# Kernel optimization log

Measured on AMD Instinct MI355X. Metric: run time of the kernel, lower is better.

## Reference

```python
import jax, jax.numpy as jnp
import numpy as np

B, T, N, F, H, E = 8, 16, 10000, 64, 64, 1000000
M = B * N  # flattened node count per timestep
NUM_CLASSES = 3


def setup_inputs() -> dict:
    key = jax.random.key(0)
    ks = jax.random.split(key, 10)
    s = 1.0 / np.sqrt(H)
    return {
        "graph_seq": jax.random.normal(ks[0], (B, T, N, F), dtype=jnp.float32),
        "edge_index_seq": jax.random.randint(ks[1], (T, 2, E), 0, M, dtype=jnp.int32),
        "W_gcn": jax.random.normal(ks[2], (F, H), dtype=jnp.float32) / np.sqrt(F),
        "b_gcn": jnp.zeros((H,), dtype=jnp.float32),
        "W_ih": jax.random.uniform(ks[3], (4 * H, H), jnp.float32, -s, s),
        "W_hh": jax.random.uniform(ks[4], (4 * H, H), jnp.float32, -s, s),
        "b_ih": jax.random.uniform(ks[5], (4 * H,), jnp.float32, -s, s),
        "b_hh": jax.random.uniform(ks[6], (4 * H,), jnp.float32, -s, s),
        "W_fc": jax.random.uniform(ks[7], (NUM_CLASSES, H), jnp.float32, -s, s),
        "b_fc": jax.random.uniform(ks[8], (NUM_CLASSES,), jnp.float32, -s, s),
    }


def _forward(graph_seq, edge_index_seq, W_gcn, b_gcn, W_ih, W_hh, b_ih, b_hh, W_fc, b_fc):
    # GCNConv: x' = D^{-1/2}(A+I)D^{-1/2} (x W) + b, applied on flattened (B*N) nodes per timestep.
    xw = jnp.einsum('btnf,fh->btnh', graph_seq, W_gcn)        # [B,T,N,H]
    xw_t = xw.transpose(1, 0, 2, 3).reshape(T, M, H)          # [T, B*N, H], node index = b*N + n

    def gcn_step(_, inp):
        x, ei = inp                                           # x: [M,H], ei: [2,E]
        src, dst = ei[0], ei[1]
        deg = jax.ops.segment_sum(jnp.ones((E,), x.dtype), dst, num_segments=M) + 1.0  # +1 self loop
        dinv = jax.lax.rsqrt(deg)
        coef = dinv[src] * dinv[dst]                          # [E]
        agg = jax.ops.segment_sum(x[src] * coef[:, None], dst, num_segments=M)
        out = agg + x * (dinv * dinv)[:, None] + b_gcn        # self-loop term + bias
        pooled = out.reshape(B, N, H).mean(axis=1)            # mean over nodes -> [B,H]
        return None, pooled

    _, pooled_seq = jax.lax.scan(gcn_step, None, (xw_t, edge_index_seq))  # [T,B,H]

    def lstm_step(carry, x_t):
        h, c = carry
        z = x_t @ W_ih.T + h @ W_hh.T + b_ih + b_hh           # [B,4H], gate order i,f,g,o
        i, f, g, o = jnp.split(z, 4, axis=-1)
        c = jax.nn.sigmoid(f) * c + jax.nn.sigmoid(i) * jnp.tanh(g)
        h = jax.nn.sigmoid(o) * jnp.tanh(c)
        return (h, c), None

    h0 = jnp.zeros((B, H), dtype=graph_seq.dtype)
    (h_last, _), _ = jax.lax.scan(lstm_step, (h0, h0), pooled_seq)
    return h_last @ W_fc.T + b_fc                             # [B,3]


def reference(graph_seq, edge_index_seq, W_gcn, b_gcn, W_ih, W_hh, b_ih, b_hh, W_fc, b_fc):
    return _forward(graph_seq, edge_index_seq, W_gcn, b_gcn, W_ih, W_hh, b_ih, b_hh, W_fc, b_fc)
```

## Files before the change

kernel.cpp:

```cpp
#include <hip/hip_runtime.h>
#include <hip/hip_bf16.h>

#define BB 8
#define TT 16
#define NNODE 10000
#define FF 64
#define HH 64
#define EE 1000000
#define MM 80000
#define NCLS 3

#define NCHUNK 32
#define NPC 2500
#define CAPB 36032
#define NSEG_H 16
#define HW 20000
#define NSEG_B 32
#define EPW 7816
#define WCAP 144
#define FLUSH_THR 96
#define GPAD 16

__global__ __launch_bounds__(256) void k_hist(const int* __restrict__ ei,
                                              unsigned int* __restrict__ part, int t0) {
    __shared__ unsigned int h[HW];
    int seg = blockIdx.x, tloc = blockIdx.y, tg = t0 + tloc;
    for (int i = threadIdx.x; i < HW; i += 256) h[i] = 0u;
    __syncthreads();
    const uint4* dstp = (const uint4*)(ei + (size_t)tg * 2 * EE + EE
                                       + (size_t)seg * (EE / NSEG_H));
    for (int i = threadIdx.x; i < (EE / NSEG_H) / 4; i += 256) {
        uint4 d4 = dstp[i];
        atomicAdd(&h[d4.x >> 2], 1u << ((d4.x & 3u) * 8u));
        atomicAdd(&h[d4.y >> 2], 1u << ((d4.y & 3u) * 8u));
        atomicAdd(&h[d4.z >> 2], 1u << ((d4.z & 3u) * 8u));
        atomicAdd(&h[d4.w >> 2], 1u << ((d4.w & 3u) * 8u));
    }
    __syncthreads();
    unsigned int* outp = part + ((size_t)tloc * NSEG_H + seg) * HW;
    for (int i = threadIdx.x; i < HW; i += 256) outp[i] = h[i];
}

__global__ __launch_bounds__(256) void k_mdeg(const unsigned int* __restrict__ part,
                                              float* __restrict__ dinv) {
    int w = blockIdx.x * 256 + threadIdx.x;
    int tloc = blockIdx.y;
    if (w >= HW) return;
    const unsigned int* p = part + (size_t)tloc * NSEG_H * HW;
    unsigned int s = 0;
#pragma unroll
    for (int k = 0; k < NSEG_H; k++) s += p[(size_t)k * HW + w];
    float4 r;
    r.x = rsqrtf((float)(s & 255u) + 1.0f);
    r.y = rsqrtf((float)((s >> 8) & 255u) + 1.0f);
    r.z = rsqrtf((float)((s >> 16) & 255u) + 1.0f);
    r.w = rsqrtf((float)((s >> 24) & 255u) + 1.0f);
    *(float4*)(dinv + (size_t)tloc * MM + (size_t)w * 4) = r;
}

__global__ __launch_bounds__(256) void k_part(const int* __restrict__ ei,
                                              unsigned int* __restrict__ buck,
                                              unsigned int* __restrict__ gcur, int t0) {
    __shared__ unsigned int stg[4][NCHUNK][WCAP];
    __shared__ unsigned int cur[4][NCHUNK];
    int wave = threadIdx.x >> 6, lane = threadIdx.x & 63;
    int tloc = blockIdx.y, tg = t0 + tloc;
    if (lane < NCHUNK) cur[wave][lane] = 0u;

    int wseg = blockIdx.x * 4 + wave;
    int e0 = wseg * EPW;
    int e1 = e0 + EPW; if (e1 > EE) e1 = EE;
    const uint4* src4 = (const uint4*)(ei + (size_t)tg * 2 * EE);
    const uint4* dst4 = (const uint4*)(ei + (size_t)tg * 2 * EE + EE);
    unsigned int* gc = gcur + (size_t)tloc * NCHUNK * GPAD;
    unsigned int* bk = buck + (size_t)tloc * NCHUNK * CAPB;

    int i40 = e0 >> 2, i41 = e1 >> 2;
    int nIter = (i41 - i40 + 63) >> 6;
    for (int k = 0; k < nIter; k++) {
        int i4 = i40 + k * 64 + lane;
        if (i4 < i41) {
            uint4 s4 = src4[i4];
            uint4 d4 = dst4[i4];
            unsigned int ss[4] = {s4.x, s4.y, s4.z, s4.w};
            unsigned int dd[4] = {d4.x, d4.y, d4.z, d4.w};
#pragma unroll
            for (int j = 0; j < 4; j++) {
                unsigned int ck = (unsigned int)(((unsigned long long)ss[j] * 1717987ull) >> 32);
                unsigned int so = ss[j] - ck * NPC;
                unsigned int p = atomicAdd(&cur[wave][ck], 1u);
                if (p < WCAP) stg[wave][ck][p] = (so << 17) | dd[j];
            }
        }
        unsigned int cnt = (lane < NCHUNK) ? cur[wave][lane] : 0u;
        unsigned long long mask = __ballot(cnt >= FLUSH_THR);
        while (mask) {
            int ck = __ffsll((unsigned long long)mask) - 1;
            mask &= mask - 1;
            unsigned int n = cur[wave][ck];
            if (n > WCAP) n = WCAP;
            unsigned int gp = 0;
            if (lane == 0) gp = atomicAdd(&gc[ck * GPAD], n);
            gp = (unsigned int)__shfl((int)gp, 0);
            if (gp + n <= CAPB) {
                for (unsigned int j = lane; j < n; j += 64)
                    bk[(size_t)ck * CAPB + gp + j] = stg[wave][ck][j];
            }
            if (lane == 0) cur[wave][ck] = 0u;
        }
    }
    for (int ck = 0; ck < NCHUNK; ck++) {
        unsigned int n = cur[wave][ck];
        if (n > WCAP) n = WCAP;
        if (n > 0u) {
            unsigned int gp = 0;
            if (lane == 0) gp = atomicAdd(&gc[ck * GPAD], n);
            gp = (unsigned int)__shfl((int)gp, 0);
            if (gp + n <= CAPB) {
                for (unsigned int j = lane; j < n; j += 64)
                    bk[(size_t)ck * CAPB + gp + j] = stg[wave][ck][j];
            }
        }
    }
}

__global__ __launch_bounds__(512) void k_scat(const float* __restrict__ g,
                                              const float* __restrict__ dinv,
                                              const unsigned int* __restrict__ buck,
                                              const unsigned int* __restrict__ gcur,
                                              float* __restrict__ yp, int t0) {
    __shared__ float a[NPC * BB];
    int c = blockIdx.x, tloc = blockIdx.y, tg = t0 + tloc;
    for (int i = threadIdx.x; i < NPC * BB; i += 512) a[i] = 0.0f;
    __syncthreads();

    const float* dv = dinv + (size_t)tloc * MM;
    unsigned int n = gcur[((size_t)tloc * NCHUNK + c) * GPAD];
    if (n > CAPB) n = CAPB;
    const unsigned int* bk = buck + ((size_t)tloc * NCHUNK + c) * CAPB;

    unsigned int n4 = n >> 2;
    for (unsigned int i = threadIdx.x; i < n4; i += 512) {
        uint4 r = ((const uint4*)bk)[i];
        unsigned int rec[4] = {r.x, r.y, r.z, r.w};
#pragma unroll
        for (int k = 0; k < 4; k++) {
            unsigned int d = rec[k] & 0x1FFFFu;
            unsigned int so = rec[k] >> 17;
            unsigned int b = (unsigned int)(((unsigned long long)d * 429497ull) >> 32);
            atomicAdd(&a[so * BB + b], dv[d]);
        }
    }
    {
        unsigned int i = (n4 << 2) + threadIdx.x;
        if (i < n) {
            unsigned int rec = bk[i];
            unsigned int d = rec & 0x1FFFFu;
            unsigned int so = rec >> 17;
            unsigned int b = (unsigned int)(((unsigned long long)d * 429497ull) >> 32);
            atomicAdd(&a[so * BB + b], dv[d]);
        }
    }
    __syncthreads();

    int lane = threadIdx.x & 63;
    int wave = threadIdx.x >> 6;
    int sub = lane >> 4;
    int f0 = (lane & 15) << 2;
    int b_c = c >> 2;
    const size_t base_g = ((size_t)(b_c * TT + tg) * NNODE + (size_t)(c & 3) * NPC) * FF;
    const float* dvc = dv + (size_t)c * NPC;

    float acc[BB][4];
#pragma unroll
    for (int b = 0; b < BB; b++)
#pragma unroll
        for (int q = 0; q < 4; q++) acc[b][q] = 0.0f;

    const int NG = NPC / 4;
    for (int gi = wave; gi < NG; gi += 16) {
        int j0 = gi * 4 + sub;
        int gi1 = gi + 8;
        int j1 = gi1 * 4 + sub;
        bool has1 = (gi1 < NG);
        const float4 g40 = *(const float4*)(g + base_g + (size_t)j0 * FF + f0);
        float4 g41 = has1 ? *(const float4*)(g + base_g + (size_t)j1 * FF + f0)
                          : make_float4(0.f, 0.f, 0.f, 0.f);
        {
            float dvj = dvc[j0];
            const float4 a0 = *(const float4*)(&a[j0 * BB]);
            const float4 a1 = *(const float4*)(&a[j0 * BB + 4]);
            float av[BB] = {a0.x, a0.y, a0.z, a0.w, a1.x, a1.y, a1.z, a1.w};
#pragma unroll
            for (int b = 0; b < BB; b++) {
                float wv = dvj * (av[b] + (b == b_c ? dvj : 0.0f));
                acc[b][0] = fmaf(g40.x, wv, acc[b][0]);
                acc[b][1] = fmaf(g40.y, wv, acc[b][1]);
                acc[b][2] = fmaf(g40.z, wv, acc[b][2]);
                acc[b][3] = fmaf(g40.w, wv, acc[b][3]);
            }
        }
        if (has1) {
            float dvj = dvc[j1];
            const float4 a0 = *(const float4*)(&a[j1 * BB]);
            const float4 a1 = *(const float4*)(&a[j1 * BB + 4]);
            float av[BB] = {a0.x, a0.y, a0.z, a0.w, a1.x, a1.y, a1.z, a1.w};
#pragma unroll
            for (int b = 0; b < BB; b++) {
                float wv = dvj * (av[b] + (b == b_c ? dvj : 0.0f));
                acc[b][0] = fmaf(g41.x, wv, acc[b][0]);
                acc[b][1] = fmaf(g41.y, wv, acc[b][1]);
                acc[b][2] = fmaf(g41.z, wv, acc[b][2]);
                acc[b][3] = fmaf(g41.w, wv, acc[b][3]);
            }
        }
    }

    __syncthreads();
#pragma unroll
    for (int b = 0; b < BB; b++)
#pragma unroll
        for (int q = 0; q < 4; q++) {
            float v = acc[b][q];
            v += __shfl_xor(v, 16);
            v += __shfl_xor(v, 32);
            acc[b][q] = v;
        }
    if (sub == 0) {
#pragma unroll
        for (int b = 0; b < BB; b++)
#pragma unroll
            for (int q = 0; q < 4; q++)
                a[wave * (BB * FF) + b * FF + f0 + q] = acc[b][q];
    }
    __syncthreads();
    for (int idx = threadIdx.x; idx < BB * FF; idx += 512) {
        float s = 0.0f;
#pragma unroll
        for (int w = 0; w < 8; w++) s += a[w * (BB * FF) + idx];
        yp[((size_t)tg * NCHUNK + c) * (BB * FF) + idx] = s;
    }
}

__global__ __launch_bounds__(256) void k_lstm(const float* __restrict__ yp,
                                              const float* __restrict__ Wg,
                                              const float* __restrict__ bg,
                                              const float* __restrict__ Wih,
                                              const float* __restrict__ Whh,
                                              const float* __restrict__ bih,
                                              const float* __restrict__ bhh,
                                              const float* __restrict__ Wfc,
                                              const float* __restrict__ bfc,
                                              float* __restrict__ out) {
    int b = blockIdx.x;
    int r = threadIdx.x;

    __shared__ float ys[TT][FF];
    __shared__ float xs[TT][HH];
    __shared__ float hs[HH], cs[HH], zs[4 * HH];

    for (int idx = r; idx < TT * FF; idx += 256) {
        int t = idx >> 6, f = idx & 63;
        const float* p = yp + ((size_t)t * NCHUNK * BB + b) * FF + f;
        float s = 0.0f;
#pragma unroll
        for (int c = 0; c < NCHUNK; c++) s += p[(size_t)c * BB * FF];
        ys[t][f] = s;
    }
    __syncthreads();

    for (int idx = r; idx < TT * HH; idx += 256) {
        int t = idx >> 6, h = idx & 63;
        float s = 0.0f;
#pragma unroll
        for (int f = 0; f < FF; f++) s = fmaf(ys[t][f], Wg[f * HH + h], s);
        xs[t][h] = s * (1.0f / NNODE) + bg[h];
    }

    float wih[HH], whh[HH];
#pragma unroll
    for (int k = 0; k < HH; k++) {
        wih[k] = Wih[r * HH + k];
        whh[k] = Whh[r * HH + k];
    }
    float bias = bih[r] + bhh[r];

    if (r < HH) { hs[r] = 0.0f; cs[r] = 0.0f; }
    __syncthreads();

    for (int t = 0; t < TT; t++) {
        float acc = bias;
#pragma unroll
        for (int k = 0; k < HH; k++)
            acc = fmaf(wih[k], xs[t][k], fmaf(whh[k], hs[k], acc));
        zs[r] = acc;
        __syncthreads();
        if (r < HH) {
            float iv = zs[r], fv = zs[HH + r], gv = zs[2 * HH + r], ov = zs[3 * HH + r];
            float si = 1.0f / (1.0f + expf(-iv));
            float sf = 1.0f / (1.0f + expf(-fv));
            float so = 1.0f / (1.0f + expf(-ov));
            float cc = sf * cs[r] + si * tanhf(gv);
            cs[r] = cc;
            hs[r] = so * tanhf(cc);
        }
        __syncthreads();
    }

    if (r < NCLS) {
        float s = bfc[r];
#pragma unroll
        for (int k = 0; k < HH; k++) s = fmaf(hs[k], Wfc[r * HH + k], s);
        out[b * NCLS + r] = s;
    }
}

extern "C" void kernel_launch(void* const* d_in, const int* in_sizes, int n_in,
                              void* d_out, int out_size, void* d_ws, size_t ws_size,
                              hipStream_t stream) {
    const float* g   = (const float*)d_in[0];
    const int*   ei  = (const int*)d_in[1];
    const float* Wg  = (const float*)d_in[2];
    const float* bg  = (const float*)d_in[3];
    const float* Wih = (const float*)d_in[4];
    const float* Whh = (const float*)d_in[5];
    const float* bih = (const float*)d_in[6];
    const float* bhh = (const float*)d_in[7];
    const float* Wfc = (const float*)d_in[8];
    const float* bfc = (const float*)d_in[9];
    float* out = (float*)d_out;

    char* ws = (char*)d_ws;
    float* yp = (float*)ws;
    const size_t ypBytes = (size_t)TT * NCHUNK * BB * FF * sizeof(float);

    const size_t sz_dinv = (size_t)MM * 4;
    const size_t sz_part = (size_t)NSEG_H * HW * 4;
    const size_t sz_buck = (size_t)NCHUNK * CAPB * 4;
    const size_t sz_gcur = (size_t)NCHUNK * GPAD * 4;
    const size_t per_t = sz_dinv + sz_part + sz_buck + sz_gcur;

    size_t avail = (ws_size > ypBytes) ? ws_size - ypBytes : 0;
    int Tg = (int)(avail / per_t);
    if (Tg > TT) Tg = TT;
    if (Tg < 1) Tg = 1;

    float* dinv        = (float*)(ws + ypBytes);
    unsigned int* part = (unsigned int*)(ws + ypBytes + (size_t)Tg * sz_dinv);
    unsigned int* buck = (unsigned int*)(ws + ypBytes + (size_t)Tg * (sz_dinv + sz_part));
    unsigned int* gcur = (unsigned int*)(ws + ypBytes + (size_t)Tg * (sz_dinv + sz_part + sz_buck));

    for (int t0 = 0; t0 < TT; t0 += Tg) {
        int tc = (TT - t0 < Tg) ? (TT - t0) : Tg;
        hipMemsetAsync(gcur, 0, (size_t)tc * NCHUNK * GPAD * 4, stream);

        dim3 gh(NSEG_H, tc);
        k_hist<<<gh, 256, 0, stream>>>(ei, part, t0);

        dim3 gm((HW + 255) / 256, tc);
        k_mdeg<<<gm, 256, 0, stream>>>(part, dinv);

        dim3 gp(NSEG_B, tc);
        k_part<<<gp, 256, 0, stream>>>(ei, buck, gcur, t0);

        dim3 gs(NCHUNK, tc);
        k_scat<<<gs, 512, 0, stream>>>(g, dinv, buck, gcur, yp, t0);
    }

    k_lstm<<<BB, 256, 0, stream>>>(yp, Wg, bg, Wih, Whh, bih, bhh, Wfc, bfc, out);
}
```

Measured before the change: 341.8 us.

## Split scatter kernel into per-chunk build and finer-grained reduction kernels

The fused scatter kernel is split in two. k_build accumulates per-chunk coefficient tables in shared memory and writes them to a global workspace. k_red then runs NCHUNK*SPLIT smaller blocks, each streaming a 500-node slice of the feature tensor against its slice of the table, which raises the block count for the bandwidth-bound reduction. In exchange it adds an extra kernel launch and a global round-trip of the coefficient tables, and the LSTM prologue has more partial sums to reduce.

```diff
diff --git a/kernel.cpp b/kernel.cpp
--- a/kernel.cpp
+++ b/kernel.cpp
@@ -20,6 +20,9 @@
 #define WCAP 144
 #define FLUSH_THR 96
 #define GPAD 16
+#define SPLIT 5
+#define RPB 500
+#define NCS (NCHUNK * SPLIT)
 
 __global__ __launch_bounds__(256) void k_hist(const int* __restrict__ ei,
                                               unsigned int* __restrict__ part, int t0) {
@@ -124,13 +127,12 @@
     }
 }
 
-__global__ __launch_bounds__(512) void k_scat(const float* __restrict__ g,
-                                              const float* __restrict__ dinv,
-                                              const unsigned int* __restrict__ buck,
-                                              const unsigned int* __restrict__ gcur,
-                                              float* __restrict__ yp, int t0) {
+__global__ __launch_bounds__(512) void k_build(const float* __restrict__ dinv,
+                                               const unsigned int* __restrict__ buck,
+                                               const unsigned int* __restrict__ gcur,
+                                               float* __restrict__ ag, int t0) {
     __shared__ float a[NPC * BB];
-    int c = blockIdx.x, tloc = blockIdx.y, tg = t0 + tloc;
+    int c = blockIdx.x, tloc = blockIdx.y;
     for (int i = threadIdx.x; i < NPC * BB; i += 512) a[i] = 0.0f;
     __syncthreads();
 
@@ -163,13 +165,35 @@
     }
     __syncthreads();
 
+    float4* agp = (float4*)(ag + ((size_t)tloc * NCHUNK + c) * NPC * BB);
+    for (int i = threadIdx.x; i < NPC * BB / 4; i += 512)
+        agp[i] = ((const float4*)a)[i];
+}
+
+__global__ __launch_bounds__(256) void k_red(const float* __restrict__ g,
+                                             const float* __restrict__ dinv,
+                                             const float* __restrict__ ag,
+                                             float* __restrict__ yp, int t0) {
+    __shared__ float as_[RPB * BB];
+    __shared__ float dvs[RPB];
+    int u = blockIdx.x;
+    int c = u / SPLIT, s = u - c * SPLIT;
+    int tloc = blockIdx.y, tg = t0 + tloc;
+
+    const float* agp = ag + (((size_t)tloc * NCHUNK + c) * NPC + (size_t)s * RPB) * BB;
+    for (int i = threadIdx.x; i < RPB * BB / 4; i += 256)
+        ((float4*)as_)[i] = ((const float4*)agp)[i];
+    const float* dvp = dinv + (size_t)tloc * MM + c * NPC + s * RPB;
+    for (int i = threadIdx.x; i < RPB; i += 256) dvs[i] = dvp[i];
+    __syncthreads();
+
     int lane = threadIdx.x & 63;
     int wave = threadIdx.x >> 6;
     int sub = lane >> 4;
     int f0 = (lane & 15) << 2;
     int b_c = c >> 2;
-    const size_t base_g = ((size_t)(b_c * TT + tg) * NNODE + (size_t)(c & 3) * NPC) * FF;
-    const float* dvc = dv + (size_t)c * NPC;
+    const size_t base_g = ((size_t)(b_c * TT + tg) * NNODE
+                           + (size_t)(c & 3) * NPC + (size_t)s * RPB) * FF;
 
     float acc[BB][4];
 #pragma unroll
@@ -177,19 +201,19 @@
 #pragma unroll
         for (int q = 0; q < 4; q++) acc[b][q] = 0.0f;
 
-    const int NG = NPC / 4;
-    for (int gi = wave; gi < NG; gi += 16) {
+    const int NG = RPB / 4;
+    for (int gi = wave; gi < NG; gi += 8) {
         int j0 = gi * 4 + sub;
-        int gi1 = gi + 8;
+        int gi1 = gi + 4;
         int j1 = gi1 * 4 + sub;
         bool has1 = (gi1 < NG);
         const float4 g40 = *(const float4*)(g + base_g + (size_t)j0 * FF + f0);
         float4 g41 = has1 ? *(const float4*)(g + base_g + (size_t)j1 * FF + f0)
                           : make_float4(0.f, 0.f, 0.f, 0.f);
         {
-            float dvj = dvc[j0];
-            const float4 a0 = *(const float4*)(&a[j0 * BB]);
-            const float4 a1 = *(const float4*)(&a[j0 * BB + 4]);
+            float dvj = dvs[j0];
+            const float4 a0 = *(const float4*)(&as_[j0 * BB]);
+            const float4 a1 = *(const float4*)(&as_[j0 * BB + 4]);
             float av[BB] = {a0.x, a0.y, a0.z, a0.w, a1.x, a1.y, a1.z, a1.w};
 #pragma unroll
             for (int b = 0; b < BB; b++) {
@@ -201,9 +225,9 @@
             }
         }
         if (has1) {
-            float dvj = dvc[j1];
-            const float4 a0 = *(const float4*)(&a[j1 * BB]);
-            const float4 a1 = *(const float4*)(&a[j1 * BB + 4]);
+            float dvj = dvs[j1];
+            const float4 a0 = *(const float4*)(&as_[j1 * BB]);
+            const float4 a1 = *(const float4*)(&as_[j1 * BB + 4]);
             float av[BB] = {a0.x, a0.y, a0.z, a0.w, a1.x, a1.y, a1.z, a1.w};
 #pragma unroll
             for (int b = 0; b < BB; b++) {
@@ -231,14 +255,12 @@
         for (int b = 0; b < BB; b++)
 #pragma unroll
             for (int q = 0; q < 4; q++)
-                a[wave * (BB * FF) + b * FF + f0 + q] = acc[b][q];
-    }
-    __syncthreads();
-    for (int idx = threadIdx.x; idx < BB * FF; idx += 512) {
-        float s = 0.0f;
-#pragma unroll
-        for (int w = 0; w < 8; w++) s += a[w * (BB * FF) + idx];
-        yp[((size_t)tg * NCHUNK + c) * (BB * FF) + idx] = s;
+                as_[wave * (BB * FF) + b * FF + f0 + q] = acc[b][q];
+    }
+    __syncthreads();
+    for (int idx = threadIdx.x; idx < BB * FF; idx += 256) {
+        float sv = as_[idx] + as_[BB * FF + idx] + as_[2 * BB * FF + idx] + as_[3 * BB * FF + idx];
+        yp[((size_t)tg * NCS + u) * (BB * FF) + idx] = sv;
     }
 }
 
@@ -261,10 +283,10 @@
 
     for (int idx = r; idx < TT * FF; idx += 256) {
         int t = idx >> 6, f = idx & 63;
-        const float* p = yp + ((size_t)t * NCHUNK * BB + b) * FF + f;
+        const float* p = yp + (size_t)t * NCS * BB * FF + b * FF + f;
         float s = 0.0f;
-#pragma unroll
-        for (int c = 0; c < NCHUNK; c++) s += p[(size_t)c * BB * FF];
+#pragma unroll 8
+        for (int u = 0; u < NCS; u++) s += p[(size_t)u * BB * FF];
         ys[t][f] = s;
     }
     __syncthreads();
@@ -332,23 +354,26 @@
 
     char* ws = (char*)d_ws;
     float* yp = (float*)ws;
-    const size_t ypBytes = (size_t)TT * NCHUNK * BB * FF * sizeof(float);
+    const size_t ypBytes = (size_t)TT * NCS * BB * FF * sizeof(float);
 
     const size_t sz_dinv = (size_t)MM * 4;
     const size_t sz_part = (size_t)NSEG_H * HW * 4;
     const size_t sz_buck = (size_t)NCHUNK * CAPB * 4;
     const size_t sz_gcur = (size_t)NCHUNK * GPAD * 4;
-    const size_t per_t = sz_dinv + sz_part + sz_buck + sz_gcur;
+    const size_t sz_ag   = (size_t)NCHUNK * NPC * BB * 4;
+    const size_t per_t = sz_dinv + sz_part + sz_buck + sz_gcur + sz_ag;
 
     size_t avail = (ws_size > ypBytes) ? ws_size - ypBytes : 0;
     int Tg = (int)(avail / per_t);
     if (Tg > TT) Tg = TT;
     if (Tg < 1) Tg = 1;
 
-    float* dinv        = (float*)(ws + ypBytes);
-    unsigned int* part = (unsigned int*)(ws + ypBytes + (size_t)Tg * sz_dinv);
-    unsigned int* buck = (unsigned int*)(ws + ypBytes + (size_t)Tg * (sz_dinv + sz_part));
-    unsigned int* gcur = (unsigned int*)(ws + ypBytes + (size_t)Tg * (sz_dinv + sz_part + sz_buck));
+    size_t ofs = ypBytes;
+    float* dinv        = (float*)(ws + ofs); ofs += (size_t)Tg * sz_dinv;
+    unsigned int* part = (unsigned int*)(ws + ofs); ofs += (size_t)Tg * sz_part;
+    unsigned int* buck = (unsigned int*)(ws + ofs); ofs += (size_t)Tg * sz_buck;
+    unsigned int* gcur = (unsigned int*)(ws + ofs); ofs += (size_t)Tg * sz_gcur;
+    float* ag          = (float*)(ws + ofs);
 
     for (int t0 = 0; t0 < TT; t0 += Tg) {
         int tc = (TT - t0 < Tg) ? (TT - t0) : Tg;
@@ -363,8 +388,11 @@
         dim3 gp(NSEG_B, tc);
         k_part<<<gp, 256, 0, stream>>>(ei, buck, gcur, t0);
 
-        dim3 gs(NCHUNK, tc);
-        k_scat<<<gs, 512, 0, stream>>>(g, dinv, buck, gcur, yp, t0);
+        dim3 gb(NCHUNK, tc);
+        k_build<<<gb, 512, 0, stream>>>(dinv, buck, gcur, ag, t0);
+
+        dim3 gr(NCS, tc);
+        k_red<<<gr, 256, 0, stream>>>(g, dinv, ag, yp, t0);
     }
 
     k_lstm<<<BB, 256, 0, stream>>>(yp, Wg, bg, Wih, Whh, bih, bhh, Wfc, bfc, out);
```

New measurement: 379.0 us. +10.9%, slower.

## Keep packed degree counts in LDS with rsqrt LUT and use 40 chunks

Applied to the files above, without the earlier changes.

Replaces the global float dinv array with packed byte degree counts (80KB per timestep), which each scatter block copies into LDS and decodes through a 256-entry rsqrt lookup table. This removes random global gathers of dinv during the edge scatter. The number of source chunks grows from 32 to 40 with smaller per-chunk buckets and staging, which gives more blocks per timestep. The gcur reset moves from a memset into k_mdeg, dropping one API call. The cost is a larger LDS footprint per block (about 145KB), which limits occupancy, and degrees are assumed to stay below 256.

```diff
diff --git a/kernel.cpp b/kernel.cpp
--- a/kernel.cpp
+++ b/kernel.cpp
@@ -10,15 +10,15 @@
 #define MM 80000
 #define NCLS 3
 
-#define NCHUNK 32
-#define NPC 2500
-#define CAPB 36032
+#define NCHUNK 40
+#define NPC 2000
+#define CAPB 26048
 #define NSEG_H 16
 #define HW 20000
 #define NSEG_B 32
 #define EPW 7816
-#define WCAP 144
-#define FLUSH_THR 96
+#define WCAP 96
+#define FLUSH_THR 64
 #define GPAD 16
 
 __global__ __launch_bounds__(256) void k_hist(const int* __restrict__ ei,
@@ -42,20 +42,18 @@
 }
 
 __global__ __launch_bounds__(256) void k_mdeg(const unsigned int* __restrict__ part,
-                                              float* __restrict__ dinv) {
+                                              unsigned int* __restrict__ degb,
+                                              unsigned int* __restrict__ gcur) {
+    int tloc = blockIdx.y;
+    if (blockIdx.x == 0 && threadIdx.x < NCHUNK)
+        gcur[((size_t)tloc * NCHUNK + threadIdx.x) * GPAD] = 0u;
     int w = blockIdx.x * 256 + threadIdx.x;
-    int tloc = blockIdx.y;
     if (w >= HW) return;
     const unsigned int* p = part + (size_t)tloc * NSEG_H * HW;
     unsigned int s = 0;
 #pragma unroll
     for (int k = 0; k < NSEG_H; k++) s += p[(size_t)k * HW + w];
-    float4 r;
-    r.x = rsqrtf((float)(s & 255u) + 1.0f);
-    r.y = rsqrtf((float)((s >> 8) & 255u) + 1.0f);
-    r.z = rsqrtf((float)((s >> 16) & 255u) + 1.0f);
-    r.w = rsqrtf((float)((s >> 24) & 255u) + 1.0f);
-    *(float4*)(dinv + (size_t)tloc * MM + (size_t)w * 4) = r;
+    degb[(size_t)tloc * HW + w] = s;
 }
 
 __global__ __launch_bounds__(256) void k_part(const int* __restrict__ ei,
@@ -86,7 +84,7 @@
             unsigned int dd[4] = {d4.x, d4.y, d4.z, d4.w};
 #pragma unroll
             for (int j = 0; j < 4; j++) {
-                unsigned int ck = (unsigned int)(((unsigned long long)ss[j] * 1717987ull) >> 32);
+                unsigned int ck = (unsigned int)(((unsigned long long)ss[j] * 2147484ull) >> 32);
                 unsigned int so = ss[j] - ck * NPC;
                 unsigned int p = atomicAdd(&cur[wave][ck], 1u);
                 if (p < WCAP) stg[wave][ck][p] = (so << 17) | dd[j];
@@ -125,16 +123,21 @@
 }
 
 __global__ __launch_bounds__(512) void k_scat(const float* __restrict__ g,
-                                              const float* __restrict__ dinv,
+                                              const unsigned int* __restrict__ degb,
                                               const unsigned int* __restrict__ buck,
                                               const unsigned int* __restrict__ gcur,
                                               float* __restrict__ yp, int t0) {
+    __shared__ unsigned int degw[HW];
     __shared__ float a[NPC * BB];
+    __shared__ float lut[256];
     int c = blockIdx.x, tloc = blockIdx.y, tg = t0 + tloc;
+
     for (int i = threadIdx.x; i < NPC * BB; i += 512) a[i] = 0.0f;
-    __syncthreads();
-
-    const float* dv = dinv + (size_t)tloc * MM;
+    const unsigned int* dgp = degb + (size_t)tloc * HW;
+    for (int i = threadIdx.x; i < HW; i += 512) degw[i] = dgp[i];
+    if (threadIdx.x < 256) lut[threadIdx.x] = rsqrtf((float)threadIdx.x + 1.0f);
+    __syncthreads();
+
     unsigned int n = gcur[((size_t)tloc * NCHUNK + c) * GPAD];
     if (n > CAPB) n = CAPB;
     const unsigned int* bk = buck + ((size_t)tloc * NCHUNK + c) * CAPB;
@@ -148,7 +151,8 @@
             unsigned int d = rec[k] & 0x1FFFFu;
             unsigned int so = rec[k] >> 17;
             unsigned int b = (unsigned int)(((unsigned long long)d * 429497ull) >> 32);
-            atomicAdd(&a[so * BB + b], dv[d]);
+            unsigned int dg = (degw[d >> 2] >> ((d & 3u) * 8u)) & 255u;
+            atomicAdd(&a[so * BB + b], lut[dg]);
         }
     }
     {
@@ -158,7 +162,8 @@
             unsigned int d = rec & 0x1FFFFu;
             unsigned int so = rec >> 17;
             unsigned int b = (unsigned int)(((unsigned long long)d * 429497ull) >> 32);
-            atomicAdd(&a[so * BB + b], dv[d]);
+            unsigned int dg = (degw[d >> 2] >> ((d & 3u) * 8u)) & 255u;
+            atomicAdd(&a[so * BB + b], lut[dg]);
         }
     }
     __syncthreads();
@@ -167,9 +172,10 @@
     int wave = threadIdx.x >> 6;
     int sub = lane >> 4;
     int f0 = (lane & 15) << 2;
-    int b_c = c >> 2;
-    const size_t base_g = ((size_t)(b_c * TT + tg) * NNODE + (size_t)(c & 3) * NPC) * FF;
-    const float* dvc = dv + (size_t)c * NPC;
+    int b_c = c / 5;
+    int coff = c - b_c * 5;
+    const size_t base_g = ((size_t)(b_c * TT + tg) * NNODE + (size_t)coff * NPC) * FF;
+    const int jbase = c * NPC;
 
     float acc[BB][4];
 #pragma unroll
@@ -187,7 +193,8 @@
         float4 g41 = has1 ? *(const float4*)(g + base_g + (size_t)j1 * FF + f0)
                           : make_float4(0.f, 0.f, 0.f, 0.f);
         {
-            float dvj = dvc[j0];
+            int jg = jbase + j0;
+            float dvj = lut[(degw[jg >> 2] >> ((jg & 3) * 8)) & 255u];
             const float4 a0 = *(const float4*)(&a[j0 * BB]);
             const float4 a1 = *(const float4*)(&a[j0 * BB + 4]);
             float av[BB] = {a0.x, a0.y, a0.z, a0.w, a1.x, a1.y, a1.z, a1.w};
@@ -201,7 +208,8 @@
             }
         }
         if (has1) {
-            float dvj = dvc[j1];
+            int jg = jbase + j1;
+            float dvj = lut[(degw[jg >> 2] >> ((jg & 3) * 8)) & 255u];
             const float4 a0 = *(const float4*)(&a[j1 * BB]);
             const float4 a1 = *(const float4*)(&a[j1 * BB + 4]);
             float av[BB] = {a0.x, a0.y, a0.z, a0.w, a1.x, a1.y, a1.z, a1.w};
@@ -261,10 +269,10 @@
 
     for (int idx = r; idx < TT * FF; idx += 256) {
         int t = idx >> 6, f = idx & 63;
-        const float* p = yp + ((size_t)t * NCHUNK * BB + b) * FF + f;
+        const float* p = yp + (size_t)t * NCHUNK * BB * FF + b * FF + f;
         float s = 0.0f;
-#pragma unroll
-        for (int c = 0; c < NCHUNK; c++) s += p[(size_t)c * BB * FF];
+#pragma unroll 8
+        for (int u = 0; u < NCHUNK; u++) s += p[(size_t)u * BB * FF];
         ys[t][f] = s;
     }
     __syncthreads();
@@ -334,37 +342,37 @@
     float* yp = (float*)ws;
     const size_t ypBytes = (size_t)TT * NCHUNK * BB * FF * sizeof(float);
 
-    const size_t sz_dinv = (size_t)MM * 4;
     const size_t sz_part = (size_t)NSEG_H * HW * 4;
+    const size_t sz_degb = (size_t)HW * 4;
     const size_t sz_buck = (size_t)NCHUNK * CAPB * 4;
     const size_t sz_gcur = (size_t)NCHUNK * GPAD * 4;
-    const size_t per_t = sz_dinv + sz_part + sz_buck + sz_gcur;
+    const size_t per_t = sz_part + sz_degb + sz_buck + sz_gcur;
 
     size_t avail = (ws_size > ypBytes) ? ws_size - ypBytes : 0;
     int Tg = (int)(avail / per_t);
     if (Tg > TT) Tg = TT;
     if (Tg < 1) Tg = 1;
 
-    float* dinv        = (float*)(ws + ypBytes);
-    unsigned int* part = (unsigned int*)(ws + ypBytes + (size_t)Tg * sz_dinv);
-    unsigned int* buck = (unsigned int*)(ws + ypBytes + (size_t)Tg * (sz_dinv + sz_part));
-    unsigned int* gcur = (unsigned int*)(ws + ypBytes + (size_t)Tg * (sz_dinv + sz_part + sz_buck));
+    size_t ofs = ypBytes;
+    unsigned int* part = (unsigned int*)(ws + ofs); ofs += (size_t)Tg * sz_part;
+    unsigned int* degb = (unsigned int*)(ws + ofs); ofs += (size_t)Tg * sz_degb;
+    unsigned int* buck = (unsigned int*)(ws + ofs); ofs += (size_t)Tg * sz_buck;
+    unsigned int* gcur = (unsigned int*)(ws + ofs);
 
     for (int t0 = 0; t0 < TT; t0 += Tg) {
         int tc = (TT - t0 < Tg) ? (TT - t0) : Tg;
-        hipMemsetAsync(gcur, 0, (size_t)tc * NCHUNK * GPAD * 4, stream);
 
         dim3 gh(NSEG_H, tc);
         k_hist<<<gh, 256, 0, stream>>>(ei, part, t0);
 
         dim3 gm((HW + 255) / 256, tc);
-        k_mdeg<<<gm, 256, 0, stream>>>(part, dinv);
+        k_mdeg<<<gm, 256, 0, stream>>>(part, degb, gcur);
 
         dim3 gp(NSEG_B, tc);
         k_part<<<gp, 256, 0, stream>>>(ei, buck, gcur, t0);
 
         dim3 gs(NCHUNK, tc);
-        k_scat<<<gs, 512, 0, stream>>>(g, dinv, buck, gcur, yp, t0);
+        k_scat<<<gs, 512, 0, stream>>>(g, degb, buck, gcur, yp, t0);
     }
 
     k_lstm<<<BB, 256, 0, stream>>>(yp, Wg, bg, Wih, Whh, bih, bhh, Wfc, bfc, out);
```

New measurement: 405.5 us. +18.6%, slower.
